# Kernel tuning notes

Hardware: AMD Instinct MI355X
Metric: run time of the kernel (lower is better)

The kernel has to match this reference:

```python
import jax, jax.numpy as jnp
import numpy as np
from math import sqrt

D_MODEL = 1024
HEADS = 16
D_K = D_MODEL // HEADS
NEG = -1e9


def setup_inputs() -> dict:
    key = jax.random.key(0)
    ks = jax.random.split(key, 8)
    bs, s, d = 2, 2048, D_MODEL
    inp = {
        "k": jax.random.normal(ks[0], (bs, s, d), jnp.float32),
        "v": jax.random.normal(ks[1], (bs, s, d), jnp.float32),
        "q": jax.random.normal(ks[2], (bs, s, d), jnp.float32),
        "mask": jax.random.randint(ks[3], (bs, s, 1), 0, 2).astype(jnp.int64),
        # torch nn.Linear weights: y = x @ W.T, W is [out, in]
        "Wq": jax.random.normal(ks[4], (d, d), jnp.float32) / sqrt(d),
        "Wk": jax.random.normal(ks[5], (d, d), jnp.float32) / sqrt(d),
        "Wv": jax.random.normal(ks[6], (d, d), jnp.float32) / sqrt(d),
        "Wo": jax.random.normal(ks[7], (d, d), jnp.float32) / sqrt(d),
    }
    return inp


def reference(k, v, q, mask, Wq, Wk, Wv, Wo):
    bs, s_k, d = k.shape
    s_q = q.shape[1]
    h, d_k = HEADS, D_K
    # linear projections (no bias), then split heads -> [bs, h, s, d_k]
    kh = (k @ Wk.T).reshape(bs, s_k, h, d_k).transpose(0, 2, 1, 3)
    vh = (v @ Wv.T).reshape(bs, s_k, h, d_k).transpose(0, 2, 1, 3)
    qh = (q @ Wq.T).reshape(bs, s_q, h, d_k).transpose(0, 2, 1, 3)
    # scaled dot-product scores [bs, h, s_q, s_k]
    scores = jnp.einsum("bhqd,bhkd->bhqk", qh, kh) / sqrt(d_k)
    # mask [bs, s_k, 1] -> [bs, 1, 1, s_k], masked positions get -1e9
    m = mask[:, None].transpose(0, 1, 3, 2)  # [bs,1,1,s_k]
    scores = jnp.where(m == 0, NEG, scores)
    probs = jax.nn.softmax(scores, axis=-1)  # dropout is identity (eval)
    attn = jnp.einsum("bhqk,bhkd->bhqd", probs, vh)
    attn_concat = attn.transpose(0, 2, 1, 3).reshape(bs, s_q, d)
    return attn_concat @ Wo.T
```

## Files before the change

### kernel.cpp

```cpp
#include <hip/hip_runtime.h>

typedef __bf16 bf16x8 __attribute__((ext_vector_type(8)));
typedef float f32x4 __attribute__((ext_vector_type(4)));

#define BS 2
#define SEQ 2048
#define DM 1024
#define NH 16
#define DKH 64
#define GM 4096
#define GN 1024
#define GK 1024
#define NEGV (-1e9f)

#define OFF_XQ 0u
#define OFF_XK 4194304u
#define OFF_XV 8388608u
#define OFF_WQ 12582912u
#define OFF_WK 13631488u
#define OFF_WV 14680064u
#define OFF_WO 15728640u
#define OFF_QH 16777216u
#define OFF_KC 20971520u
#define OFF_VT 25165824u
#define OFF_AT OFF_XQ

#if __has_builtin(__builtin_amdgcn_exp2f)
#define EXP2(x) __builtin_amdgcn_exp2f(x)
#else
static __device__ __forceinline__ float EXP2(float x) {
    float r;
    asm volatile("v_exp_f32 %0, %1" : "=v"(r) : "v"(x));
    return r;
}
#endif

__device__ __forceinline__ unsigned cvt_pk(float lo, float hi) {
    unsigned r;
    asm volatile("v_cvt_pk_bf16_f32 %0, %1, %2" : "=v"(r) : "v"(lo), "v"(hi));
    return r;
}

__device__ __forceinline__ unsigned short f2b(float f) {
    unsigned u = __builtin_bit_cast(unsigned, f);
    u += 0x7fffu + ((u >> 16) & 1u);
    return (unsigned short)(u >> 16);
}

typedef const __attribute__((address_space(1))) unsigned int* gas_t;
typedef __attribute__((address_space(3))) unsigned int* las_t;

__device__ __forceinline__ void gload_lds16(const ushort* g, ushort* l) {
    __builtin_amdgcn_global_load_lds((gas_t)(const void*)g, (las_t)(void*)l, 16, 0, 0);
}

#define BARRIER() __builtin_amdgcn_s_barrier()
#define VMCNT(n) asm volatile("s_waitcnt vmcnt(" #n ")" ::: "memory")

__global__ __launch_bounds__(256)
void cvt_scan(const float* __restrict__ q, const float* __restrict__ k,
              const float* __restrict__ v, const float* __restrict__ wq,
              const float* __restrict__ wk, const float* __restrict__ wv,
              const float* __restrict__ wo, ushort* __restrict__ ws,
              const int* __restrict__ mask, int* __restrict__ cpos,
              int* __restrict__ mbuf)
{
    const int tid = threadIdx.x;
    if (blockIdx.y == 7) {
        if (blockIdx.x >= 2) return;
        const int b = blockIdx.x;
        const int* mp = mask + (size_t)b * SEQ;
        const int lane = tid & 63, w = tid >> 6;
        int vv[8];
        int cnt = 0;
#pragma unroll
        for (int j = 0; j < 8; ++j) { vv[j] = mp[tid * 8 + j]; cnt += (vv[j] != 0); }
        int inc = cnt;
#pragma unroll
        for (int d = 1; d < 64; d <<= 1) {
            int t = __shfl_up(inc, d);
            if (lane >= d) inc += t;
        }
        __shared__ int wsum[4];
        if (lane == 63) wsum[w] = inc;
        __syncthreads();
        int base = inc - cnt;
        for (int i = 0; i < w; ++i) base += wsum[i];
        int c = base;
        int* ob = cpos + (size_t)b * SEQ;
#pragma unroll
        for (int j = 0; j < 8; ++j) {
            ob[tid * 8 + j] = (vv[j] != 0) ? c : -1;
            c += (vv[j] != 0);
        }
        if (tid == 255) mbuf[b] = base + cnt;
        return;
    }
    const float* src; unsigned n; unsigned dst;
    switch (blockIdx.y) {
        case 0: src = q;  n = 4194304u; dst = OFF_XQ; break;
        case 1: src = k;  n = 4194304u; dst = OFF_XK; break;
        case 2: src = v;  n = 4194304u; dst = OFF_XV; break;
        case 3: src = wq; n = 1048576u; dst = OFF_WQ; break;
        case 4: src = wk; n = 1048576u; dst = OFF_WK; break;
        case 5: src = wv; n = 1048576u; dst = OFF_WV; break;
        default: src = wo; n = 1048576u; dst = OFF_WO; break;
    }
    unsigned i = (blockIdx.x * 256u + tid) * 8u;
    if (i >= n) return;
    float4 f0 = *(const float4*)(src + i);
    float4 f1 = *(const float4*)(src + i + 4);
    uint4 o;
    o.x = cvt_pk(f0.x, f0.y);
    o.y = cvt_pk(f0.z, f0.w);
    o.z = cvt_pk(f1.x, f1.y);
    o.w = cvt_pk(f1.z, f1.w);
    *(uint4*)(ws + dst + i) = o;
}

__global__ __launch_bounds__(512)
void gemm256(const ushort* __restrict__ Abase, const ushort* __restrict__ Bbase,
             ushort* __restrict__ wsbase, const int* __restrict__ cpos)
{
    __shared__ __align__(16) ushort lA[2][2][8192];
    __shared__ __align__(16) ushort lB[2][2][8192];

    const unsigned z = blockIdx.z;
    const ushort* A  = Abase + (size_t)z * (GM * GK);
    const ushort* Bw = Bbase + (size_t)z * (GN * GK);
    const float scale = (z == 0) ? 0.125f * 1.44269504088896f : 1.0f;

    const int tid = threadIdx.x;
    const int lane = tid & 63, wid = tid >> 6;
    const int wr = wid >> 2, wc = wid & 3;
    const int lr = lane & 15, lg = lane >> 4;
    const int srow8 = lane >> 3, scol = lane & 7;

    const int lin = blockIdx.y * 4 + blockIdx.x;
    const int xcd = lin & 7, kidx = lin >> 3;
    const int m0 = (xcd * 2 + (kidx >> 2)) * 256;
    const int n0 = (kidx & 3) * 256;

    f32x4 acc[8][4] = {};
    bf16x8 aq[4][2], aq2[4][2], b01[2][2], b23[2][2];

#define STAGE_A(s, h, t)                                                          \
    _Pragma("unroll") for (int c = 0; c < 2; ++c) {                               \
        int rih = (wid * 2 + c) * 8 + srow8;                                      \
        gload_lds16(A + (size_t)(m0 + (h) * 128 + rih) * GK + (t) * 64 +          \
                        ((scol ^ (rih & 7)) * 8),                                 \
                    &lA[s][h][(wid * 2 + c) * 512]);                              \
    }
#define STAGE_B(s, h, t)                                                          \
    _Pragma("unroll") for (int c = 0; c < 2; ++c) {                               \
        int rih = (wid * 2 + c) * 8 + srow8;                                      \
        gload_lds16(Bw + (size_t)(n0 + (h) * 128 + rih) * GK + (t) * 64 +         \
                         ((scol ^ (rih & 7)) * 8),                                \
                    &lB[s][h][(wid * 2 + c) * 512]);                              \
    }
#define LDA_FRAG(dst, s, ibase)                                                   \
    _Pragma("unroll") for (int i2 = 0; i2 < 4; ++i2)                              \
    _Pragma("unroll") for (int kk = 0; kk < 2; ++kk) {                            \
        int row = ((ibase) + i2) * 16 + lr;                                       \
        dst[i2][kk] = *(const bf16x8*)&lA[s][wr][row * 64 +                       \
                          (((kk * 4 + lg) ^ (row & 7)) * 8)];                     \
    }
#define LDB_FRAG(dst, s, jbase)                                                   \
    _Pragma("unroll") for (int j2 = 0; j2 < 2; ++j2)                              \
    _Pragma("unroll") for (int kk = 0; kk < 2; ++kk) {                            \
        int row = (wc & 1) * 64 + ((jbase) + j2) * 16 + lr;                       \
        dst[j2][kk] = *(const bf16x8*)&lB[s][wc >> 1][row * 64 +                  \
                          (((kk * 4 + lg) ^ (row & 7)) * 8)];                     \
    }
#define MMA_Q(ibase, jbase, av, bv)                                               \
    __builtin_amdgcn_s_setprio(1);                                                \
    _Pragma("unroll") for (int i2 = 0; i2 < 4; ++i2)                              \
    _Pragma("unroll") for (int j2 = 0; j2 < 2; ++j2)                              \
    _Pragma("unroll") for (int kk = 0; kk < 2; ++kk)                              \
        acc[(ibase) + i2][(jbase) + j2] = __builtin_amdgcn_mfma_f32_16x16x32_bf16(\
            av[i2][kk], bv[j2][kk], acc[(ibase) + i2][(jbase) + j2], 0, 0, 0);    \
    __builtin_amdgcn_s_setprio(0);

    STAGE_B(0, 0, 0); STAGE_B(0, 1, 0); STAGE_A(0, 0, 0); STAGE_A(0, 1, 0);
    STAGE_B(1, 0, 1); STAGE_B(1, 1, 1); STAGE_A(1, 0, 1); STAGE_A(1, 1, 1);
    VMCNT(8);
    BARRIER();

    for (int it = 0; it < 7; ++it) {
        const int t2 = 2 * it + 2, t3 = 2 * it + 3;
        LDA_FRAG(aq, 0, 0); LDB_FRAG(b01, 0, 0); LDB_FRAG(b23, 0, 2);
        BARRIER();
        MMA_Q(0, 0, aq, b01); MMA_Q(0, 2, aq, b23);
        BARRIER();
        LDA_FRAG(aq2, 0, 4);
        STAGE_B(0, 0, t2); STAGE_B(0, 1, t2); STAGE_A(0, 0, t2); STAGE_A(0, 1, t2);
        VMCNT(8);
        BARRIER();
        MMA_Q(4, 2, aq2, b23); MMA_Q(4, 0, aq2, b01);
        BARRIER();
        LDA_FRAG(aq, 1, 0); LDB_FRAG(b01, 1, 0); LDB_FRAG(b23, 1, 2);
        BARRIER();
        MMA_Q(0, 0, aq, b01); MMA_Q(0, 2, aq, b23);
        BARRIER();
        LDA_FRAG(aq2, 1, 4);
        STAGE_B(1, 0, t3); STAGE_B(1, 1, t3); STAGE_A(1, 0, t3); STAGE_A(1, 1, t3);
        VMCNT(8);
        BARRIER();
        MMA_Q(4, 2, aq2, b23); MMA_Q(4, 0, aq2, b01);
        BARRIER();
    }

    LDA_FRAG(aq, 0, 0); LDB_FRAG(b01, 0, 0); LDB_FRAG(b23, 0, 2);
    BARRIER();
    MMA_Q(0, 0, aq, b01); MMA_Q(0, 2, aq, b23);
    BARRIER();
    LDA_FRAG(aq2, 0, 4);
    VMCNT(0);
    BARRIER();
    MMA_Q(4, 2, aq2, b23); MMA_Q(4, 0, aq2, b01);
    BARRIER();
    LDA_FRAG(aq, 1, 0); LDB_FRAG(b01, 1, 0); LDB_FRAG(b23, 1, 2);
    BARRIER();
    MMA_Q(0, 0, aq, b01); MMA_Q(0, 2, aq, b23);
    BARRIER();
    LDA_FRAG(aq2, 1, 4);
    BARRIER();
    MMA_Q(4, 2, aq2, b23); MMA_Q(4, 0, aq2, b01);
    BARRIER();

    ushort* qh  = wsbase + OFF_QH;
    ushort* kc  = wsbase + OFF_KC;
    ushort* vtp = wsbase + OFF_VT;
#pragma unroll
    for (int i = 0; i < 8; ++i) {
#pragma unroll
        for (int r = 0; r < 4; ++r) {
            int row = m0 + wr * 128 + i * 16 + lg * 4 + r;
            int b = row >> 11, s = row & 2047;
            if (z == 0) {
#pragma unroll
                for (int j = 0; j < 4; ++j) {
                    int col = n0 + wc * 64 + j * 16 + lr;
                    qh[(((size_t)b * NH + (col >> 6)) * SEQ + s) * DKH + (col & 63)] =
                        f2b(acc[i][j][r] * scale);
                }
            } else {
                int c = cpos[b * SEQ + s];
                if (c >= 0) {
                    if (z == 1) {
#pragma unroll
                        for (int j = 0; j < 4; ++j) {
                            int col = n0 + wc * 64 + j * 16 + lr;
                            kc[(((size_t)b * NH + (col >> 6)) * SEQ + c) * DKH + (col & 63)] =
                                f2b(acc[i][j][r]);
                        }
                    } else {
                        int vt = (c & ~63) | ((c & 15) * 4 + ((c >> 4) & 3));
#pragma unroll
                        for (int j = 0; j < 4; ++j) {
                            int col = n0 + wc * 64 + j * 16 + lr;
                            vtp[(((size_t)b * NH + (col >> 6)) * DKH + (col & 63)) * SEQ + vt] =
                                f2b(acc[i][j][r]);
                        }
                    }
                }
            }
        }
    }
#undef STAGE_A
#undef STAGE_B
#undef LDA_FRAG
#undef LDB_FRAG
#undef MMA_Q
}

__global__ __launch_bounds__(256)
void gemm_bt(const ushort* __restrict__ A, const ushort* __restrict__ Bw,
             float* __restrict__ of)
{
    __shared__ __align__(16) ushort lA[2][128 * 64];
    __shared__ __align__(16) ushort lB[2][128 * 64];

    const int tid = threadIdx.x;
    const int lane = tid & 63, wid = tid >> 6;
    const int wr = wid >> 1, wc = wid & 1;
    const int lr = lane & 15, lg = lane >> 4;
    const int lin = blockIdx.y * 8 + blockIdx.x;
    const int swz = (lin & 7) * 32 + (lin >> 3);
    const int m0 = (swz >> 3) * 128, n0 = (swz & 7) * 128;
    const int srow8 = lane >> 3, scol = lane & 7;

    f32x4 acc[4][4] = {};
    bf16x8 af[2][4], bfr[2][4];

#define OSTAGE(s, t)                                                               \
    _Pragma("unroll") for (int p = 0; p < 4; ++p) {                                \
        int r = wid * 32 + p * 8 + srow8;                                          \
        gload_lds16(A + (size_t)(m0 + r) * GK + (t) * 64 + ((scol ^ (r & 7)) * 8), \
                    &lA[s][(wid * 32 + p * 8) * 64]);                              \
        gload_lds16(Bw + (size_t)(n0 + r) * GK + (t) * 64 + ((scol ^ (r & 7)) * 8),\
                    &lB[s][(wid * 32 + p * 8) * 64]);                              \
    }
#define OLDX(s)                                                                    \
    _Pragma("unroll") for (int kk = 0; kk < 2; ++kk)                               \
    _Pragma("unroll") for (int i = 0; i < 4; ++i) {                                \
        int ra = wr * 64 + i * 16 + lr;                                            \
        af[kk][i] = *(const bf16x8*)&lA[s][ra * 64 + (((kk * 4 + lg) ^ (ra & 7)) * 8)];  \
        int rb = wc * 64 + i * 16 + lr;                                            \
        bfr[kk][i] = *(const bf16x8*)&lB[s][rb * 64 + (((kk * 4 + lg) ^ (rb & 7)) * 8)]; \
    }
#define OMMA()                                                                     \
    __builtin_amdgcn_s_setprio(1);                                                 \
    _Pragma("unroll") for (int kk = 0; kk < 2; ++kk)                               \
    _Pragma("unroll") for (int i = 0; i < 4; ++i)                                  \
    _Pragma("unroll") for (int j = 0; j < 4; ++j)                                  \
        acc[i][j] = __builtin_amdgcn_mfma_f32_16x16x32_bf16(af[kk][i], bfr[kk][j], \
                                                            acc[i][j], 0, 0, 0);   \
    __builtin_amdgcn_s_setprio(0);

    OSTAGE(0, 0);
    __syncthreads();

    for (int t = 0; t < 16; ++t) {
        const int cur = t & 1;
        if (t + 1 < 16) OSTAGE(cur ^ 1, t + 1);
        OLDX(cur);
        OMMA();
        __syncthreads();
    }

#pragma unroll
    for (int i = 0; i < 4; ++i)
#pragma unroll
        for (int j = 0; j < 4; ++j) {
            int col = n0 + wc * 64 + j * 16 + lr;
#pragma unroll
            for (int r = 0; r < 4; ++r) {
                int row = m0 + wr * 64 + i * 16 + lg * 4 + r;
                of[(size_t)row * GN + col] = acc[i][j][r];
            }
        }
#undef OSTAGE
#undef OLDX
#undef OMMA
}

__global__ __launch_bounds__(256)
void attn_kernel(ushort* __restrict__ ws, const int* __restrict__ mbuf)
{
    const int bid = blockIdx.x;
    const int qt = bid & 15;
    const int h  = (bid >> 4) & 15;
    const int b  = bid >> 8;
    const int bh = b * NH + h;

    const ushort* Qp = ws + OFF_QH + (size_t)bh * (SEQ * DKH);
    const ushort* Kc = ws + OFF_KC + (size_t)bh * (SEQ * DKH);
    const ushort* VT = ws + OFF_VT + (size_t)bh * (DKH * SEQ);
    ushort* At = ws + OFF_AT;

    const int mb = mbuf[b];
    const int nt = (mb + 63) >> 6;

    __shared__ __align__(16) ushort lK[3][64 * 64];
    __shared__ __align__(16) ushort lV[3][64 * 64];
    __shared__ __align__(16) ushort lP[4][32][72];

    const int tid = threadIdx.x;
    const int lane = tid & 63, wid = tid >> 6;
    const int lr = lane & 15, lg = lane >> 4;
    ushort* lPw = &lP[wid][0][0];

    const int srow = wid * 16 + (lane >> 3);
    const int sg = lane & 7;

    const int qrow0 = qt * 128 + wid * 32;
    bf16x8 qf[2][2];
#pragma unroll
    for (int fr = 0; fr < 2; ++fr)
#pragma unroll
        for (int kk = 0; kk < 2; ++kk)
            qf[fr][kk] = *(const bf16x8*)(Qp + (size_t)(qrow0 + fr * 16 + lr) * DKH + kk * 32 + lg * 8);

    f32x4 acc_o[2][4] = {};
    float lrun[2][4] = {};

    auto STAGE = [&](int buf, int kt) {
        const int kbase = kt * 64;
#pragma unroll
        for (int c = 0; c < 2; ++c) {
            int r = srow + c * 8;
            gload_lds16(Kc + (size_t)(kbase + r) * DKH + ((sg ^ (r & 7)) * 8),
                        &lK[buf][(wid * 16 + c * 8) * 64]);
            gload_lds16(VT + (size_t)r * SEQ + kbase + ((sg ^ (r & 7)) * 8),
                        &lV[buf][(wid * 16 + c * 8) * 64]);
        }
    };

    STAGE(0, 0);
    if (nt > 1) STAGE(1, 1);

    int slot = 0;
    for (int kt = 0; kt < nt; ++kt) {
        if (kt + 1 < nt) { VMCNT(4); } else { VMCNT(0); }
        BARRIER();
        if (kt + 2 < nt) {
            int s2 = slot + 2; if (s2 >= 3) s2 -= 3;
            STAGE(s2, kt + 2);
        }
        const ushort* lKc = lK[slot];
        const ushort* lVc = lV[slot];

        f32x4 s[2][4];
        __builtin_amdgcn_s_setprio(1);
#pragma unroll
        for (int fc = 0; fc < 4; ++fc) {
            int row = fc * 16 + lr;
            int sw = row & 7;
            bf16x8 kf0 = *(const bf16x8*)(lKc + row * 64 + ((lg ^ sw) * 8));
            bf16x8 kf1 = *(const bf16x8*)(lKc + row * 64 + (((4 + lg) ^ sw) * 8));
#pragma unroll
            for (int fr = 0; fr < 2; ++fr) {
                f32x4 t = {};
                t = __builtin_amdgcn_mfma_f32_16x16x32_bf16(qf[fr][0], kf0, t, 0, 0, 0);
                t = __builtin_amdgcn_mfma_f32_16x16x32_bf16(qf[fr][1], kf1, t, 0, 0, 0);
                s[fr][fc] = t;
            }
        }
        __builtin_amdgcn_s_setprio(0);

        if (kt == nt - 1) {
            const int kbase = kt * 64;
#pragma unroll
            for (int fc = 0; fc < 4; ++fc)
                if (kbase + fc * 16 + lr >= mb)
#pragma unroll
                    for (int fr = 0; fr < 2; ++fr)
                        s[fr][fc] = f32x4{NEGV, NEGV, NEGV, NEGV};
        }

#pragma unroll
        for (int fr = 0; fr < 2; ++fr)
#pragma unroll
            for (int r = 0; r < 4; ++r) {
                float p0 = EXP2(s[fr][0][r]), p1 = EXP2(s[fr][1][r]);
                float p2 = EXP2(s[fr][2][r]), p3 = EXP2(s[fr][3][r]);
                lrun[fr][r] += (p0 + p1) + (p2 + p3);
                uint2 pk;
                pk.x = cvt_pk(p0, p1);
                pk.y = cvt_pk(p2, p3);
                *(uint2*)(lPw + (fr * 16 + lg * 4 + r) * 72 + lr * 4) = pk;
            }

        __builtin_amdgcn_s_setprio(1);
#pragma unroll
        for (int kk = 0; kk < 2; ++kk) {
            bf16x8 pf[2];
#pragma unroll
            for (int fr = 0; fr < 2; ++fr)
                pf[fr] = *(const bf16x8*)(lPw + (fr * 16 + lr) * 72 + kk * 32 + lg * 8);
#pragma unroll
            for (int fc2 = 0; fc2 < 4; ++fc2) {
                int d = fc2 * 16 + lr;
                bf16x8 vf = *(const bf16x8*)(lVc + d * 64 + (((kk * 4 + lg) ^ (d & 7)) * 8));
#pragma unroll
                for (int fr = 0; fr < 2; ++fr)
                    acc_o[fr][fc2] = __builtin_amdgcn_mfma_f32_16x16x32_bf16(pf[fr], vf, acc_o[fr][fc2], 0, 0, 0);
            }
        }
        __builtin_amdgcn_s_setprio(0);

        ++slot; if (slot >= 3) slot -= 3;
    }

#pragma unroll
    for (int fr = 0; fr < 2; ++fr)
#pragma unroll
        for (int r = 0; r < 4; ++r) {
            float l = lrun[fr][r];
            l += __shfl_xor(l, 1);
            l += __shfl_xor(l, 2);
            l += __shfl_xor(l, 4);
            l += __shfl_xor(l, 8);
            float rl = 1.0f / l;
            int qrow = qrow0 + fr * 16 + lg * 4 + r;
#pragma unroll
            for (int fc2 = 0; fc2 < 4; ++fc2)
                At[((size_t)(b * SEQ) + qrow) * DM + h * DKH + fc2 * 16 + lr] =
                    f2b(acc_o[fr][fc2][r] * rl);
        }
}

extern "C" void kernel_launch(void* const* d_in, const int* in_sizes, int n_in,
                              void* d_out, int out_size, void* d_ws, size_t ws_size,
                              hipStream_t stream) {
    const float* kin = (const float*)d_in[0];
    const float* vin = (const float*)d_in[1];
    const float* qin = (const float*)d_in[2];
    const int*   msk = (const int*)d_in[3];
    const float* wq  = (const float*)d_in[4];
    const float* wk  = (const float*)d_in[5];
    const float* wv  = (const float*)d_in[6];
    const float* wo  = (const float*)d_in[7];
    ushort* ws = (ushort*)d_ws;
    float* out = (float*)d_out;
    int* cposb = (int*)d_out;
    int* mbuf = cposb + BS * SEQ;

    cvt_scan<<<dim3(2048, 8), 256, 0, stream>>>(qin, kin, vin, wq, wk, wv, wo,
                                                ws, msk, cposb, mbuf);
    gemm256<<<dim3(4, 16, 3), 512, 0, stream>>>(ws + OFF_XQ, ws + OFF_WQ, ws, cposb);
    attn_kernel<<<512, 256, 0, stream>>>(ws, mbuf);
    gemm_bt<<<dim3(8, 32), 256, 0, stream>>>(ws + OFF_AT, ws + OFF_WO, out);
}
```

Measured before the change: 120.1 us.

## Restructure QKV projection GEMM into barrier-free per-wave 64x64 tiles

The fused QKV projection GEMM goes from 192 blocks of 512 threads, each computing a shared 256x256 tile with many block barriers, to 768 blocks of 256 threads. Each wave now computes its own 64x64 tile from a private double-buffered LDS region and waits only on its own loads with vmcnt, so no block barriers are needed. The aim is to fill more CUs, since 192 blocks do not cover all of them, and to drop synchronisation stalls. The cost is lower data reuse: B rows are loaded separately by each of the four waves, and the block now uses 128KB of LDS, which limits occupancy.

```diff
diff --git a/kernel.cpp b/kernel.cpp
--- a/kernel.cpp
+++ b/kernel.cpp
@@ -118,129 +118,89 @@
     *(uint4*)(ws + dst + i) = o;
 }
 
-__global__ __launch_bounds__(512)
+__global__ __launch_bounds__(256)
 void gemm256(const ushort* __restrict__ Abase, const ushort* __restrict__ Bbase,
              ushort* __restrict__ wsbase, const int* __restrict__ cpos)
 {
-    __shared__ __align__(16) ushort lA[2][2][8192];
-    __shared__ __align__(16) ushort lB[2][2][8192];
-
-    const unsigned z = blockIdx.z;
+    __shared__ __align__(16) ushort pool[4][2][2][4096];
+
+    const unsigned z = blockIdx.y;
     const ushort* A  = Abase + (size_t)z * (GM * GK);
     const ushort* Bw = Bbase + (size_t)z * (GN * GK);
     const float scale = (z == 0) ? 0.125f * 1.44269504088896f : 1.0f;
 
     const int tid = threadIdx.x;
     const int lane = tid & 63, wid = tid >> 6;
-    const int wr = wid >> 2, wc = wid & 3;
     const int lr = lane & 15, lg = lane >> 4;
-    const int srow8 = lane >> 3, scol = lane & 7;
-
-    const int lin = blockIdx.y * 4 + blockIdx.x;
-    const int xcd = lin & 7, kidx = lin >> 3;
-    const int m0 = (xcd * 2 + (kidx >> 2)) * 256;
-    const int n0 = (kidx & 3) * 256;
-
-    f32x4 acc[8][4] = {};
-    bf16x8 aq[4][2], aq2[4][2], b01[2][2], b23[2][2];
-
-#define STAGE_A(s, h, t)                                                          \
-    _Pragma("unroll") for (int c = 0; c < 2; ++c) {                               \
-        int rih = (wid * 2 + c) * 8 + srow8;                                      \
-        gload_lds16(A + (size_t)(m0 + (h) * 128 + rih) * GK + (t) * 64 +          \
-                        ((scol ^ (rih & 7)) * 8),                                 \
-                    &lA[s][h][(wid * 2 + c) * 512]);                              \
-    }
-#define STAGE_B(s, h, t)                                                          \
-    _Pragma("unroll") for (int c = 0; c < 2; ++c) {                               \
-        int rih = (wid * 2 + c) * 8 + srow8;                                      \
-        gload_lds16(Bw + (size_t)(n0 + (h) * 128 + rih) * GK + (t) * 64 +         \
-                         ((scol ^ (rih & 7)) * 8),                                \
-                    &lB[s][h][(wid * 2 + c) * 512]);                              \
-    }
-#define LDA_FRAG(dst, s, ibase)                                                   \
-    _Pragma("unroll") for (int i2 = 0; i2 < 4; ++i2)                              \
-    _Pragma("unroll") for (int kk = 0; kk < 2; ++kk) {                            \
-        int row = ((ibase) + i2) * 16 + lr;                                       \
-        dst[i2][kk] = *(const bf16x8*)&lA[s][wr][row * 64 +                       \
-                          (((kk * 4 + lg) ^ (row & 7)) * 8)];                     \
-    }
-#define LDB_FRAG(dst, s, jbase)                                                   \
-    _Pragma("unroll") for (int j2 = 0; j2 < 2; ++j2)                              \
-    _Pragma("unroll") for (int kk = 0; kk < 2; ++kk) {                            \
-        int row = (wc & 1) * 64 + ((jbase) + j2) * 16 + lr;                       \
-        dst[j2][kk] = *(const bf16x8*)&lB[s][wc >> 1][row * 64 +                  \
-                          (((kk * 4 + lg) ^ (row & 7)) * 8)];                     \
-    }
-#define MMA_Q(ibase, jbase, av, bv)                                               \
-    __builtin_amdgcn_s_setprio(1);                                                \
-    _Pragma("unroll") for (int i2 = 0; i2 < 4; ++i2)                              \
-    _Pragma("unroll") for (int j2 = 0; j2 < 2; ++j2)                              \
-    _Pragma("unroll") for (int kk = 0; kk < 2; ++kk)                              \
-        acc[(ibase) + i2][(jbase) + j2] = __builtin_amdgcn_mfma_f32_16x16x32_bf16(\
-            av[i2][kk], bv[j2][kk], acc[(ibase) + i2][(jbase) + j2], 0, 0, 0);    \
-    __builtin_amdgcn_s_setprio(0);
-
-    STAGE_B(0, 0, 0); STAGE_B(0, 1, 0); STAGE_A(0, 0, 0); STAGE_A(0, 1, 0);
-    STAGE_B(1, 0, 1); STAGE_B(1, 1, 1); STAGE_A(1, 0, 1); STAGE_A(1, 1, 1);
-    VMCNT(8);
-    BARRIER();
-
-    for (int it = 0; it < 7; ++it) {
-        const int t2 = 2 * it + 2, t3 = 2 * it + 3;
-        LDA_FRAG(aq, 0, 0); LDB_FRAG(b01, 0, 0); LDB_FRAG(b23, 0, 2);
-        BARRIER();
-        MMA_Q(0, 0, aq, b01); MMA_Q(0, 2, aq, b23);
-        BARRIER();
-        LDA_FRAG(aq2, 0, 4);
-        STAGE_B(0, 0, t2); STAGE_B(0, 1, t2); STAGE_A(0, 0, t2); STAGE_A(0, 1, t2);
-        VMCNT(8);
-        BARRIER();
-        MMA_Q(4, 2, aq2, b23); MMA_Q(4, 0, aq2, b01);
-        BARRIER();
-        LDA_FRAG(aq, 1, 0); LDB_FRAG(b01, 1, 0); LDB_FRAG(b23, 1, 2);
-        BARRIER();
-        MMA_Q(0, 0, aq, b01); MMA_Q(0, 2, aq, b23);
-        BARRIER();
-        LDA_FRAG(aq2, 1, 4);
-        STAGE_B(1, 0, t3); STAGE_B(1, 1, t3); STAGE_A(1, 0, t3); STAGE_A(1, 1, t3);
-        VMCNT(8);
-        BARRIER();
-        MMA_Q(4, 2, aq2, b23); MMA_Q(4, 0, aq2, b01);
-        BARRIER();
-    }
-
-    LDA_FRAG(aq, 0, 0); LDB_FRAG(b01, 0, 0); LDB_FRAG(b23, 0, 2);
-    BARRIER();
-    MMA_Q(0, 0, aq, b01); MMA_Q(0, 2, aq, b23);
-    BARRIER();
-    LDA_FRAG(aq2, 0, 4);
-    VMCNT(0);
-    BARRIER();
-    MMA_Q(4, 2, aq2, b23); MMA_Q(4, 0, aq2, b01);
-    BARRIER();
-    LDA_FRAG(aq, 1, 0); LDB_FRAG(b01, 1, 0); LDB_FRAG(b23, 1, 2);
-    BARRIER();
-    MMA_Q(0, 0, aq, b01); MMA_Q(0, 2, aq, b23);
-    BARRIER();
-    LDA_FRAG(aq2, 1, 4);
-    BARRIER();
-    MMA_Q(4, 2, aq2, b23); MMA_Q(4, 0, aq2, b01);
-    BARRIER();
+    const int grow = lane >> 3, gseg = lane & 7;
+
+    const int lin = blockIdx.x;
+    const int xcd = lin & 7, kid = lin >> 3;
+    const int mi = xcd * 2 + (kid >> 4), ni = kid & 15;
+    const int m0 = mi * 256 + wid * 64;
+    const int n0 = ni * 64;
+
+    ushort* lA[2] = { &pool[wid][0][0][0], &pool[wid][1][0][0] };
+    ushort* lB[2] = { &pool[wid][0][1][0], &pool[wid][1][1][0] };
+
+    f32x4 acc[4][4] = {};
+
+    auto STAGE = [&](int s, int t) {
+        const int k0 = t * 64;
+#pragma unroll
+        for (int g = 0; g < 8; ++g) {
+            int row = g * 8 + grow;
+            gload_lds16(A + (size_t)(m0 + row) * GK + k0 + ((gseg ^ (row & 7)) * 8),
+                        lA[s] + g * 512);
+            gload_lds16(Bw + (size_t)(n0 + row) * GK + k0 + ((gseg ^ (row & 7)) * 8),
+                        lB[s] + g * 512);
+        }
+    };
+
+    STAGE(0, 0);
+    STAGE(1, 1);
+
+    for (int t = 0; t < 16; ++t) {
+        const int s = t & 1;
+        if (t < 15) { VMCNT(16); } else { VMCNT(0); }
+        const ushort* la = lA[s];
+        const ushort* lb = lB[s];
+        bf16x8 af[2][4], bfr[2][4];
+#pragma unroll
+        for (int kk = 0; kk < 2; ++kk)
+#pragma unroll
+            for (int i = 0; i < 4; ++i) {
+                int ra = i * 16 + lr;
+                int off = ra * 64 + (((kk * 4 + lg) ^ (ra & 7)) * 8);
+                af[kk][i]  = *(const bf16x8*)&la[off];
+                bfr[kk][i] = *(const bf16x8*)&lb[off];
+            }
+        __builtin_amdgcn_s_setprio(1);
+#pragma unroll
+        for (int kk = 0; kk < 2; ++kk)
+#pragma unroll
+            for (int i = 0; i < 4; ++i)
+#pragma unroll
+                for (int j = 0; j < 4; ++j)
+                    acc[i][j] = __builtin_amdgcn_mfma_f32_16x16x32_bf16(
+                        af[kk][i], bfr[kk][j], acc[i][j], 0, 0, 0);
+        __builtin_amdgcn_s_setprio(0);
+        if (t + 2 < 16) STAGE(s, t + 2);
+    }
 
     ushort* qh  = wsbase + OFF_QH;
     ushort* kc  = wsbase + OFF_KC;
     ushort* vtp = wsbase + OFF_VT;
 #pragma unroll
-    for (int i = 0; i < 8; ++i) {
+    for (int i = 0; i < 4; ++i) {
 #pragma unroll
         for (int r = 0; r < 4; ++r) {
-            int row = m0 + wr * 128 + i * 16 + lg * 4 + r;
+            int row = m0 + i * 16 + lg * 4 + r;
             int b = row >> 11, s = row & 2047;
             if (z == 0) {
 #pragma unroll
                 for (int j = 0; j < 4; ++j) {
-                    int col = n0 + wc * 64 + j * 16 + lr;
+                    int col = n0 + j * 16 + lr;
                     qh[(((size_t)b * NH + (col >> 6)) * SEQ + s) * DKH + (col & 63)] =
                         f2b(acc[i][j][r] * scale);
                 }
@@ -250,7 +210,7 @@
                     if (z == 1) {
 #pragma unroll
                         for (int j = 0; j < 4; ++j) {
-                            int col = n0 + wc * 64 + j * 16 + lr;
+                            int col = n0 + j * 16 + lr;
                             kc[(((size_t)b * NH + (col >> 6)) * SEQ + c) * DKH + (col & 63)] =
                                 f2b(acc[i][j][r]);
                         }
@@ -258,7 +218,7 @@
                         int vt = (c & ~63) | ((c & 15) * 4 + ((c >> 4) & 3));
 #pragma unroll
                         for (int j = 0; j < 4; ++j) {
-                            int col = n0 + wc * 64 + j * 16 + lr;
+                            int col = n0 + j * 16 + lr;
                             vtp[(((size_t)b * NH + (col >> 6)) * DKH + (col & 63)) * SEQ + vt] =
                                 f2b(acc[i][j][r]);
                         }
@@ -267,11 +227,6 @@
             }
         }
     }
-#undef STAGE_A
-#undef STAGE_B
-#undef LDA_FRAG
-#undef LDB_FRAG
-#undef MMA_Q
 }
 
 __global__ __launch_bounds__(256)
@@ -509,7 +464,7 @@
 
     cvt_scan<<<dim3(2048, 8), 256, 0, stream>>>(qin, kin, vin, wq, wk, wv, wo,
                                                 ws, msk, cposb, mbuf);
-    gemm256<<<dim3(4, 16, 3), 512, 0, stream>>>(ws + OFF_XQ, ws + OFF_WQ, ws, cposb);
+    gemm256<<<dim3(256, 3), 256, 0, stream>>>(ws + OFF_XQ, ws + OFF_WQ, ws, cposb);
     attn_kernel<<<512, 256, 0, stream>>>(ws, mbuf);
     gemm_bt<<<dim3(8, 32), 256, 0, stream>>>(ws + OFF_AT, ws + OFF_WO, out);
 }
```

Result: faster. 116.8 us, median of 2 (-2.7%).
